# Performance work log

Hardware: AMD Instinct MI355X
Metric: run time of the kernel (lower is better)

The kernel has to match this reference:

```python
import jax, jax.numpy as jnp
import numpy as np

K, C, W, PAD, B = 64, 64, 128, 4, 16  # faces processed, channels, face width, pad, batch
W2 = W + 2 * PAD


def setup_inputs() -> dict:
    key = jax.random.key(0)
    k1, k2, k3, k4, k5, k6 = jax.random.split(key, 6)
    cube = jax.random.normal(k1, (K, C, W, W), dtype=jnp.float32)
    # to_process: sorted unique subset of faces from the 6*B face pool
    to_process = jnp.sort(jax.random.permutation(k2, 6 * B)[:K]).astype(jnp.int32)
    pixel_idx_tb = jax.random.randint(k3, (6, C, 2 * PAD, W2), 0, C * W * W, dtype=jnp.int32)
    pixel_idx_lr = jax.random.randint(k4, (6, C, W, 2 * PAD), 0, C * W * W, dtype=jnp.int32)
    face_idx_tb = jax.random.randint(k5, (6, 2 * PAD, W2), 0, 6, dtype=jnp.int32)
    face_idx_lr = jax.random.randint(k6, (6, W, 2 * PAD), 0, 6, dtype=jnp.int32)
    return {
        "cube": cube,
        "to_process": to_process,
        "batch_size": B,
        "pixel_idx_tb": pixel_idx_tb,
        "pixel_idx_lr": pixel_idx_lr,
        "face_idx_tb": face_idx_tb,
        "face_idx_lr": face_idx_lr,
    }


def reference(cube, to_process, batch_size, pixel_idx_tb, pixel_idx_lr, face_idx_tb, face_idx_lr):
    k, c, w, _ = cube.shape
    p = PAD
    # inverse map: global face id -> row in cube, -1 if not processed
    inv = jnp.full((6 * batch_size,), -1, dtype=jnp.int32).at[to_process].set(
        jnp.arange(k, dtype=jnp.int32))
    flat_cube = cube.reshape(-1)  # (k*c*w*w,)

    def pad_block(face_idx, pixel_idx):
        # face_idx: (6, *sp), pixel_idx: (6, c, *sp)
        f = face_idx[None] + 6 * jnp.arange(batch_size, dtype=jnp.int32).reshape(-1, 1, 1, 1)
        f = f.reshape((6 * batch_size,) + face_idx.shape[1:])[to_process]  # (k, *sp)
        f = inv[f]  # -1 where neighbor face not processed
        px = pixel_idx[to_process % 6]  # (k, c, *sp)
        idx = f[:, None] * (c * w * w) + px  # (k, c, *sp)
        mask = idx >= 0
        g = jnp.take(flat_cube, jnp.maximum(idx, 0), axis=0)
        return jnp.where(mask, g, jnp.zeros((), cube.dtype))

    pad_tb = pad_block(face_idx_tb, pixel_idx_tb)  # (k, c, 2p, w+2p)
    pad_lr = pad_block(face_idx_lr, pixel_idx_lr)  # (k, c, w, 2p)

    padded = jnp.concatenate([pad_lr[:, :, :, :p], cube, pad_lr[:, :, :, p:]], axis=3)
    padded = jnp.concatenate([pad_tb[:, :, :p, :], padded, pad_tb[:, :, p:, :]], axis=2)
    return padded  # (k, c, w+2p, w+2p)
```

## Files before the change

kernel.cpp:

```cpp
#include <hip/hip_runtime.h>

#define K_   64
#define C_   64
#define W_   128
#define P_   4
#define B_   16
#define W2_  (W_ + 2*P_)
#define OUTSP (W2_*W2_)
#define CWW  (C_*W_*W_)

__global__ void interior_copy_kernel(const float4* __restrict__ cube4,
                                     float* __restrict__ out) {
    const int n4 = K_ * C_ * W_ * (W_ / 4);
    for (int t = blockIdx.x * blockDim.x + threadIdx.x; t < n4;
         t += gridDim.x * blockDim.x) {
        int q  = t & 31;
        int R  = t >> 5;
        int r  = R & (W_ - 1);
        int kc = R >> 7;
        float4 v = cube4[t];
        float4* dst = reinterpret_cast<float4*>(
            out + (size_t)kc * OUTSP + (size_t)(r + P_) * W2_ + P_) + q;
        *dst = v;
    }
}

__global__ void pad_tb_kernel(const float* __restrict__ flat_cube,
                              const int* __restrict__ to_process,
                              const int* __restrict__ pixel_idx_tb,
                              const int* __restrict__ face_idx_tb,
                              float* __restrict__ out) {
    __shared__ int inv[6 * B_];
    __shared__ int tp[K_];
    const int tid = threadIdx.x;
    if (tid < 6 * B_) inv[tid] = -1;
    if (tid < K_)     tp[tid]  = to_process[tid];
    __syncthreads();
    if (tid < K_)     inv[tp[tid]] = tid;
    __syncthreads();

    const int NT = K_ * C_ * (2 * P_) * W2_;
    for (int t = blockIdx.x * blockDim.x + tid; t < NT;
         t += gridDim.x * blockDim.x) {
        int col  = t % W2_;
        int rest = t / W2_;
        int rr   = rest % (2 * P_);
        rest    /= (2 * P_);
        int cc   = rest % C_;
        int kk   = rest / C_;

        int g  = tp[kk];
        int b  = g / 6;
        int fb = g - 6 * b;
        int nbr = face_idx_tb[(fb * 2 * P_ + rr) * W2_ + col] + 6 * b;
        int f   = inv[nbr];
        int px  = pixel_idx_tb[((fb * C_ + cc) * 2 * P_ + rr) * W2_ + col];
        float v = 0.0f;
        if (f >= 0) v = flat_cube[(size_t)f * CWW + px];

        int outr = (rr < P_) ? rr : (W_ + rr);
        out[(size_t)(kk * C_ + cc) * OUTSP + (size_t)outr * W2_ + col] = v;
    }
}

__global__ void pad_lr_kernel(const float* __restrict__ flat_cube,
                              const int* __restrict__ to_process,
                              const int* __restrict__ pixel_idx_lr,
                              const int* __restrict__ face_idx_lr,
                              float* __restrict__ out) {
    __shared__ int inv[6 * B_];
    __shared__ int tp[K_];
    const int tid = threadIdx.x;
    if (tid < 6 * B_) inv[tid] = -1;
    if (tid < K_)     tp[tid]  = to_process[tid];
    __syncthreads();
    if (tid < K_)     inv[tp[tid]] = tid;
    __syncthreads();

    const int NT = K_ * C_ * W_ * (2 * P_);
    for (int t = blockIdx.x * blockDim.x + tid; t < NT;
         t += gridDim.x * blockDim.x) {
        int j    = t % (2 * P_);
        int rest = t / (2 * P_);
        int r    = rest % W_;
        rest    /= W_;
        int cc   = rest % C_;
        int kk   = rest / C_;

        int g  = tp[kk];
        int b  = g / 6;
        int fb = g - 6 * b;
        int nbr = face_idx_lr[(fb * W_ + r) * 2 * P_ + j] + 6 * b;
        int f   = inv[nbr];
        int px  = pixel_idx_lr[((fb * C_ + cc) * W_ + r) * 2 * P_ + j];
        float v = 0.0f;
        if (f >= 0) v = flat_cube[(size_t)f * CWW + px];

        int outc = (j < P_) ? j : (W_ + j);
        out[(size_t)(kk * C_ + cc) * OUTSP + (size_t)(r + P_) * W2_ + outc] = v;
    }
}

extern "C" void kernel_launch(void* const* d_in, const int* in_sizes, int n_in,
                              void* d_out, int out_size, void* d_ws, size_t ws_size,
                              hipStream_t stream) {
    const float* cube         = (const float*)d_in[0];
    const int*   to_process   = (const int*)d_in[1];
    const int*   pixel_idx_tb = (const int*)d_in[3];
    const int*   pixel_idx_lr = (const int*)d_in[4];
    const int*   face_idx_tb  = (const int*)d_in[5];
    const int*   face_idx_lr  = (const int*)d_in[6];
    float*       out          = (float*)d_out;

    interior_copy_kernel<<<4096, 256, 0, stream>>>(
        (const float4*)cube, out);

    pad_tb_kernel<<<2048, 256, 0, stream>>>(
        cube, to_process, pixel_idx_tb, face_idx_tb, out);
    pad_lr_kernel<<<2048, 256, 0, stream>>>(
        cube, to_process, pixel_idx_lr, face_idx_lr, out);
}
```

Measured before the change: 245.0 us.

## Fuse interior copy and pad gathers into one kernel with vectorized pad paths

Merges the interior copy and the top/bottom and left/right pad gathers into a single grid-stride kernel, so three launches become one. The pad paths now handle four output elements per thread with int4 index loads and float4 stores. All output writes use nontemporal stores. This aims to cut launch overhead and per-element instruction and index-load cost, at the risk of divergence at the region boundaries and a smaller effective grid for the large interior copy.

```diff
diff --git a/kernel.cpp b/kernel.cpp
--- a/kernel.cpp
+++ b/kernel.cpp
@@ -5,31 +5,25 @@
 #define W_   128
 #define P_   4
 #define B_   16
-#define W2_  (W_ + 2*P_)
-#define OUTSP (W2_*W2_)
-#define CWW  (C_*W_*W_)
+#define W2_  136
+#define OUTSP 18496
+#define CWW  1048576
 
-__global__ void interior_copy_kernel(const float4* __restrict__ cube4,
-                                     float* __restrict__ out) {
-    const int n4 = K_ * C_ * W_ * (W_ / 4);
-    for (int t = blockIdx.x * blockDim.x + threadIdx.x; t < n4;
-         t += gridDim.x * blockDim.x) {
-        int q  = t & 31;
-        int R  = t >> 5;
-        int r  = R & (W_ - 1);
-        int kc = R >> 7;
-        float4 v = cube4[t];
-        float4* dst = reinterpret_cast<float4*>(
-            out + (size_t)kc * OUTSP + (size_t)(r + P_) * W2_ + P_) + q;
-        *dst = v;
-    }
-}
+#define N_INT 16777216
+#define N_TB  1114112
+#define N_LR  1048576
+#define N_TOT (N_INT + N_TB + N_LR)
 
-__global__ void pad_tb_kernel(const float* __restrict__ flat_cube,
-                              const int* __restrict__ to_process,
-                              const int* __restrict__ pixel_idx_tb,
-                              const int* __restrict__ face_idx_tb,
-                              float* __restrict__ out) {
+typedef int   int4n   __attribute__((ext_vector_type(4)));
+typedef float float4n __attribute__((ext_vector_type(4)));
+
+__global__ void fused_pad_kernel(const float* __restrict__ cube,
+                                 const int* __restrict__ to_process,
+                                 const int* __restrict__ px_tb,
+                                 const int* __restrict__ px_lr,
+                                 const int* __restrict__ fi_tb,
+                                 const int* __restrict__ fi_lr,
+                                 float* __restrict__ out) {
     __shared__ int inv[6 * B_];
     __shared__ int tp[K_];
     const int tid = threadIdx.x;
@@ -39,65 +33,77 @@
     if (tid < K_)     inv[tp[tid]] = tid;
     __syncthreads();
 
-    const int NT = K_ * C_ * (2 * P_) * W2_;
-    for (int t = blockIdx.x * blockDim.x + tid; t < NT;
-         t += gridDim.x * blockDim.x) {
-        int col  = t % W2_;
-        int rest = t / W2_;
-        int rr   = rest % (2 * P_);
-        rest    /= (2 * P_);
-        int cc   = rest % C_;
-        int kk   = rest / C_;
+    const int stride = gridDim.x * blockDim.x;
+    for (int t = blockIdx.x * blockDim.x + tid; t < N_TOT; t += stride) {
+        if (t < N_INT) {
+            int q  = t & 31;
+            int R  = t >> 5;
+            int r  = R & (W_ - 1);
+            int kc = R >> 7;
+            float4n v = reinterpret_cast<const float4n*>(cube)[t];
+            float4n* dst = reinterpret_cast<float4n*>(
+                out + (size_t)kc * OUTSP + (size_t)(r + P_) * W2_ + P_) + q;
+            __builtin_nontemporal_store(v, dst);
+        } else if (t < N_INT + N_TB) {
+            int u    = t - N_INT;
+            int col4 = u % 34;
+            int rest = u / 34;
+            int rr   = rest & 7;  rest >>= 3;
+            int cc   = rest & 63;
+            int kk   = rest >> 6;
 
-        int g  = tp[kk];
-        int b  = g / 6;
-        int fb = g - 6 * b;
-        int nbr = face_idx_tb[(fb * 2 * P_ + rr) * W2_ + col] + 6 * b;
-        int f   = inv[nbr];
-        int px  = pixel_idx_tb[((fb * C_ + cc) * 2 * P_ + rr) * W2_ + col];
-        float v = 0.0f;
-        if (f >= 0) v = flat_cube[(size_t)f * CWW + px];
+            int g  = tp[kk];
+            int b  = g / 6;
+            int fb = g - 6 * b;
+            int4n fiv = *reinterpret_cast<const int4n*>(
+                fi_tb + (fb * 2 * P_ + rr) * W2_ + col4 * 4);
+            int4n pxv = *reinterpret_cast<const int4n*>(
+                px_tb + (((fb * C_ + cc) * 2 * P_) + rr) * W2_ + col4 * 4);
 
-        int outr = (rr < P_) ? rr : (W_ + rr);
-        out[(size_t)(kk * C_ + cc) * OUTSP + (size_t)outr * W2_ + col] = v;
-    }
-}
+            float4n v;
+            int f0 = inv[fiv.x + 6 * b];
+            int f1 = inv[fiv.y + 6 * b];
+            int f2 = inv[fiv.z + 6 * b];
+            int f3 = inv[fiv.w + 6 * b];
+            v.x = (f0 >= 0) ? cube[(size_t)f0 * CWW + pxv.x] : 0.0f;
+            v.y = (f1 >= 0) ? cube[(size_t)f1 * CWW + pxv.y] : 0.0f;
+            v.z = (f2 >= 0) ? cube[(size_t)f2 * CWW + pxv.z] : 0.0f;
+            v.w = (f3 >= 0) ? cube[(size_t)f3 * CWW + pxv.w] : 0.0f;
 
-__global__ void pad_lr_kernel(const float* __restrict__ flat_cube,
-                              const int* __restrict__ to_process,
-                              const int* __restrict__ pixel_idx_lr,
-                              const int* __restrict__ face_idx_lr,
-                              float* __restrict__ out) {
-    __shared__ int inv[6 * B_];
-    __shared__ int tp[K_];
-    const int tid = threadIdx.x;
-    if (tid < 6 * B_) inv[tid] = -1;
-    if (tid < K_)     tp[tid]  = to_process[tid];
-    __syncthreads();
-    if (tid < K_)     inv[tp[tid]] = tid;
-    __syncthreads();
+            int outr = (rr < P_) ? rr : (W_ + rr);
+            float4n* dst = reinterpret_cast<float4n*>(
+                out + (size_t)(kk * C_ + cc) * OUTSP + (size_t)outr * W2_ + col4 * 4);
+            __builtin_nontemporal_store(v, dst);
+        } else {
+            int u  = t - N_INT - N_TB;
+            int q  = u & 1;
+            int r  = (u >> 1) & (W_ - 1);
+            int cc = (u >> 8) & 63;
+            int kk = u >> 14;
 
-    const int NT = K_ * C_ * W_ * (2 * P_);
-    for (int t = blockIdx.x * blockDim.x + tid; t < NT;
-         t += gridDim.x * blockDim.x) {
-        int j    = t % (2 * P_);
-        int rest = t / (2 * P_);
-        int r    = rest % W_;
-        rest    /= W_;
-        int cc   = rest % C_;
-        int kk   = rest / C_;
+            int g  = tp[kk];
+            int b  = g / 6;
+            int fb = g - 6 * b;
+            int4n fiv = *reinterpret_cast<const int4n*>(
+                fi_lr + (fb * W_ + r) * 2 * P_ + q * 4);
+            int4n pxv = *reinterpret_cast<const int4n*>(
+                px_lr + ((fb * C_ + cc) * W_ + r) * 2 * P_ + q * 4);
 
-        int g  = tp[kk];
-        int b  = g / 6;
-        int fb = g - 6 * b;
-        int nbr = face_idx_lr[(fb * W_ + r) * 2 * P_ + j] + 6 * b;
-        int f   = inv[nbr];
-        int px  = pixel_idx_lr[((fb * C_ + cc) * W_ + r) * 2 * P_ + j];
-        float v = 0.0f;
-        if (f >= 0) v = flat_cube[(size_t)f * CWW + px];
+            float4n v;
+            int f0 = inv[fiv.x + 6 * b];
+            int f1 = inv[fiv.y + 6 * b];
+            int f2 = inv[fiv.z + 6 * b];
+            int f3 = inv[fiv.w + 6 * b];
+            v.x = (f0 >= 0) ? cube[(size_t)f0 * CWW + pxv.x] : 0.0f;
+            v.y = (f1 >= 0) ? cube[(size_t)f1 * CWW + pxv.y] : 0.0f;
+            v.z = (f2 >= 0) ? cube[(size_t)f2 * CWW + pxv.z] : 0.0f;
+            v.w = (f3 >= 0) ? cube[(size_t)f3 * CWW + pxv.w] : 0.0f;
 
-        int outc = (j < P_) ? j : (W_ + j);
-        out[(size_t)(kk * C_ + cc) * OUTSP + (size_t)(r + P_) * W2_ + outc] = v;
+            int outc = q ? (W_ + P_) : 0;
+            float4n* dst = reinterpret_cast<float4n*>(
+                out + (size_t)(kk * C_ + cc) * OUTSP + (size_t)(r + P_) * W2_ + outc);
+            __builtin_nontemporal_store(v, dst);
+        }
     }
 }
 
@@ -112,11 +118,7 @@
     const int*   face_idx_lr  = (const int*)d_in[6];
     float*       out          = (float*)d_out;
 
-    interior_copy_kernel<<<4096, 256, 0, stream>>>(
-        (const float4*)cube, out);
-
-    pad_tb_kernel<<<2048, 256, 0, stream>>>(
-        cube, to_process, pixel_idx_tb, face_idx_tb, out);
-    pad_lr_kernel<<<2048, 256, 0, stream>>>(
-        cube, to_process, pixel_idx_lr, face_idx_lr, out);
+    fused_pad_kernel<<<2048, 256, 0, stream>>>(
+        cube, to_process, pixel_idx_tb, pixel_idx_lr,
+        face_idx_tb, face_idx_lr, out);
 }
```

Result: faster. 223.3 us (-8.9%).
